# Performance work log

Hardware: AMD Instinct MI355X
Metric: run time of the kernel (lower is better)

The kernel has to match this reference:

```python
import jax, jax.numpy as jnp
import numpy as np

EPS = 1e-5

def _bn(z, g, b):
    # train-mode BatchNorm2d: batch stats over (B,H,W), biased variance
    mean = z.mean(axis=(0, 2, 3), keepdims=True)
    var = z.var(axis=(0, 2, 3), keepdims=True)
    return g[None, :, None, None] * (z - mean) * jax.lax.rsqrt(var + EPS) + b[None, :, None, None]

def _conv1x1(x, w):
    # x: [B,C,H,W], w: [O,C] -> [B,O,H,W]
    return jnp.einsum('bchw,oc->bohw', x, w)

def _proj(x, w1, g1, b1, w2, g2, b2):
    z = _bn(_conv1x1(x, w1), g1, b1)
    return _bn(_conv1x1(z, w2), g2, b2)

def setup_inputs() -> dict:
    key = jax.random.key(0)
    ks = jax.random.split(key, 24)
    B, Cx, Cy, M, H, W = 4, 512, 256, 64, 64, 64
    f32 = jnp.float32
    def wmat(k, o, c):
        return jax.random.normal(k, (o, c), f32) * (c ** -0.5)
    def gamma(k, c):
        return 1.0 + 0.1 * jax.random.normal(k, (c,), f32)
    def beta(k, c):
        return 0.1 * jax.random.normal(k, (c,), f32)
    inp = {
        'x': jax.random.normal(ks[0], (B, Cx, H, W), f32),
        'y': jax.random.normal(ks[1], (B, Cy, H, W), f32),
        # f_self
        'ws1': wmat(ks[2], M, Cx), 'gs1': gamma(ks[3], M), 'bs1': beta(ks[4], M),
        'ws2': wmat(ks[5], M, M),  'gs2': gamma(ks[6], M), 'bs2': beta(ks[7], M),
        # f_x
        'wx1': wmat(ks[8], M, Cx), 'gx1': gamma(ks[9], M), 'bx1': beta(ks[10], M),
        'wx2': wmat(ks[11], M, M), 'gx2': gamma(ks[12], M), 'bx2': beta(ks[13], M),
        # f_y
        'wy1': wmat(ks[14], M, Cy), 'gy1': gamma(ks[15], M), 'by1': beta(ks[16], M),
        'wy2': wmat(ks[17], M, M),  'gy2': gamma(ks[18], M), 'by2': beta(ks[19], M),
        # f_up
        'wu': wmat(ks[20], Cx, M), 'gu': gamma(ks[21], Cx), 'bu': beta(ks[22], Cx),
    }
    return inp

def reference(x, y, ws1, gs1, bs1, ws2, gs2, bs2,
              wx1, gx1, bx1, wx2, gx2, bx2,
              wy1, gy1, by1, wy2, gy2, by2,
              wu, gu, bu):
    B, C, H, W = x.shape
    M = ws1.shape[0]
    N = H * W
    fself = _proj(x, ws1, gs1, bs1, ws2, gs2, bs2).reshape(B, M, N).transpose(0, 2, 1)  # [B,N,M]
    fx = _proj(x, wx1, gx1, bx1, wx2, gx2, bx2).reshape(B, M, N).transpose(0, 2, 1)      # [B,N,M]
    fy = _proj(y, wy1, gy1, by1, wy2, gy2, by2).reshape(B, M, N)                          # [B,M,N]
    sim = jnp.matmul(fx, fy)                  # [B,N,N]  (scale=False)
    attn = jax.nn.softmax(sim, axis=-1)
    fout = jnp.matmul(attn, fself)            # [B,N,M]
    fout = fout.transpose(0, 2, 1).reshape(B, M, H, W)
    out = _bn(_conv1x1(fout, wu), gu, bu)
    return x + out
```

## Files before the change

kernel.cpp:

```cpp
#include <hip/hip_runtime.h>
#include <hip/hip_fp16.h>
#include <cstdint>

constexpr int N_ = 4096;
constexpr float CNT = 16384.f;

typedef __attribute__((ext_vector_type(8))) _Float16 half8;
typedef __attribute__((ext_vector_type(4))) float f32x4;
union fragh { half8 h8; int i4[4]; };

__device__ inline int pkh(float a, float b) {
  union { __half2 h; int i; } u;
  u.h = __float22half2_rn(float2{a, b});
  return u.i;
}


__global__ __launch_bounds__(256) void conv1_k(
    const float* __restrict__ x, const float* __restrict__ y,
    const float* __restrict__ ws1, const float* __restrict__ wx1,
    const float* __restrict__ wy1,
    float* __restrict__ z1s, float* __restrict__ z1x, float* __restrict__ z1y,
    float* __restrict__ stats) {
  const int t = threadIdx.x;
  const int slice = blockIdx.x;
  const int b = slice >> 5;
  const int n0 = (slice & 31) * 128;
  const int branch = blockIdx.y;
  const float* A = branch == 2 ? y : x;
  const float* W = branch == 0 ? ws1 : (branch == 1 ? wx1 : wy1);
  float* out = branch == 0 ? z1s : (branch == 1 ? z1x : z1y);
  const int K = branch == 2 ? 256 : 512;
  float* st = stats + branch * 128;

  __shared__ float sA[32][132];
  __shared__ float sW[32][72];

  const int to = (t >> 5) * 8;
  const int tn = (t & 31) * 4;
  float acc[8][4];
#pragma unroll
  for (int i = 0; i < 8; ++i)
#pragma unroll
    for (int j = 0; j < 4; ++j) acc[i][j] = 0.f;

  const float* Ab = A + (size_t)b * K * N_ + n0;
#pragma unroll 1
  for (int k0 = 0; k0 < K; k0 += 32) {
    __syncthreads();
#pragma unroll
    for (int i = 0; i < 4; ++i) {
      int row = i * 8 + (t >> 5);
      float4 v = *(const float4*)&Ab[(size_t)(k0 + row) * N_ + tn];
      *(float4*)&sA[row][tn] = v;
    }
    {
      int o = t >> 2, kk = (t & 3) * 8;
      float4 w0 = *(const float4*)&W[(size_t)o * K + k0 + kk];
      float4 w1 = *(const float4*)&W[(size_t)o * K + k0 + kk + 4];
      sW[kk + 0][o] = w0.x; sW[kk + 1][o] = w0.y;
      sW[kk + 2][o] = w0.z; sW[kk + 3][o] = w0.w;
      sW[kk + 4][o] = w1.x; sW[kk + 5][o] = w1.y;
      sW[kk + 6][o] = w1.z; sW[kk + 7][o] = w1.w;
    }
    __syncthreads();
#pragma unroll
    for (int k = 0; k < 32; ++k) {
      float4 a = *(const float4*)&sA[k][tn];
      float4 w0 = *(const float4*)&sW[k][to];
      float4 w1 = *(const float4*)&sW[k][to + 4];
      float wv[8] = {w0.x, w0.y, w0.z, w0.w, w1.x, w1.y, w1.z, w1.w};
      float av[4] = {a.x, a.y, a.z, a.w};
#pragma unroll
      for (int i = 0; i < 8; ++i)
#pragma unroll
        for (int j = 0; j < 4; ++j) acc[i][j] += wv[i] * av[j];
    }
  }
  float* Cb = out + (size_t)b * 64 * N_ + n0;
#pragma unroll
  for (int i = 0; i < 8; ++i) {
    float4 v = {acc[i][0], acc[i][1], acc[i][2], acc[i][3]};
    *(float4*)&Cb[(size_t)(to + i) * N_ + tn] = v;
  }
#pragma unroll
  for (int i = 0; i < 8; ++i) {
    float s = acc[i][0] + acc[i][1] + acc[i][2] + acc[i][3];
    float q = acc[i][0] * acc[i][0] + acc[i][1] * acc[i][1] +
              acc[i][2] * acc[i][2] + acc[i][3] * acc[i][3];
#pragma unroll
    for (int d = 1; d < 32; d <<= 1) { s += __shfl_xor(s, d); q += __shfl_xor(q, d); }
    if ((t & 31) == 0) { atomicAdd(&st[to + i], s); atomicAdd(&st[64 + to + i], q); }
  }
}

__global__ __launch_bounds__(256) void conv2_k(
    const float* __restrict__ z1s, const float* __restrict__ z1x,
    const float* __restrict__ z1y,
    const float* __restrict__ ws2, const float* __restrict__ wx2,
    const float* __restrict__ wy2,
    const float* __restrict__ gs1, const float* __restrict__ bs1,
    const float* __restrict__ gx1, const float* __restrict__ bx1,
    const float* __restrict__ gy1, const float* __restrict__ by1,
    float* __restrict__ z2s, float* __restrict__ z2x, float* __restrict__ z2y,
    float* __restrict__ stats) {
  const int t = threadIdx.x;
  const int slice = blockIdx.x;
  const int b = slice >> 5;
  const int n0 = (slice & 31) * 128;
  const int branch = blockIdx.y;
  const float* A = branch == 0 ? z1s : (branch == 1 ? z1x : z1y);
  const float* W = branch == 0 ? ws2 : (branch == 1 ? wx2 : wy2);
  const float* g1 = branch == 0 ? gs1 : (branch == 1 ? gx1 : gy1);
  const float* b1 = branch == 0 ? bs1 : (branch == 1 ? bx1 : by1);
  float* out = branch == 0 ? z2s : (branch == 1 ? z2x : z2y);
  const float* stin = stats + branch * 128;
  float* stout = stats + (3 + branch) * 128;

  __shared__ float sA[32][132];
  __shared__ float sW[32][72];
  __shared__ float sc[64], sh[64];

  if (t < 64) {
    float mean = stin[t] * (1.f / CNT);
    float var = stin[64 + t] * (1.f / CNT) - mean * mean;
    float r = rsqrtf(var + 1e-5f);
    float s = g1[t] * r;
    sc[t] = s;
    sh[t] = b1[t] - mean * s;
  }

  const int to = (t >> 5) * 8;
  const int tn = (t & 31) * 4;
  float acc[8][4];
#pragma unroll
  for (int i = 0; i < 8; ++i)
#pragma unroll
    for (int j = 0; j < 4; ++j) acc[i][j] = 0.f;

  const float* Ab = A + (size_t)b * 64 * N_ + n0;
#pragma unroll 1
  for (int k0 = 0; k0 < 64; k0 += 32) {
    __syncthreads();
#pragma unroll
    for (int i = 0; i < 4; ++i) {
      int row = i * 8 + (t >> 5);
      float4 v = *(const float4*)&Ab[(size_t)(k0 + row) * N_ + tn];
      float s = sc[k0 + row], h = sh[k0 + row];
      v.x = v.x * s + h; v.y = v.y * s + h; v.z = v.z * s + h; v.w = v.w * s + h;
      *(float4*)&sA[row][tn] = v;
    }
    {
      int o = t >> 2, kk = (t & 3) * 8;
      float4 w0 = *(const float4*)&W[(size_t)o * 64 + k0 + kk];
      float4 w1 = *(const float4*)&W[(size_t)o * 64 + k0 + kk + 4];
      sW[kk + 0][o] = w0.x; sW[kk + 1][o] = w0.y;
      sW[kk + 2][o] = w0.z; sW[kk + 3][o] = w0.w;
      sW[kk + 4][o] = w1.x; sW[kk + 5][o] = w1.y;
      sW[kk + 6][o] = w1.z; sW[kk + 7][o] = w1.w;
    }
    __syncthreads();
#pragma unroll
    for (int k = 0; k < 32; ++k) {
      float4 a = *(const float4*)&sA[k][tn];
      float4 w0 = *(const float4*)&sW[k][to];
      float4 w1 = *(const float4*)&sW[k][to + 4];
      float wv[8] = {w0.x, w0.y, w0.z, w0.w, w1.x, w1.y, w1.z, w1.w};
      float av[4] = {a.x, a.y, a.z, a.w};
#pragma unroll
      for (int i = 0; i < 8; ++i)
#pragma unroll
        for (int j = 0; j < 4; ++j) acc[i][j] += wv[i] * av[j];
    }
  }
  float* Cb = out + (size_t)b * 64 * N_ + n0;
#pragma unroll
  for (int i = 0; i < 8; ++i) {
    float4 v = {acc[i][0], acc[i][1], acc[i][2], acc[i][3]};
    *(float4*)&Cb[(size_t)(to + i) * N_ + tn] = v;
  }
#pragma unroll
  for (int i = 0; i < 8; ++i) {
    float s = acc[i][0] + acc[i][1] + acc[i][2] + acc[i][3];
    float q = acc[i][0] * acc[i][0] + acc[i][1] * acc[i][1] +
              acc[i][2] * acc[i][2] + acc[i][3] * acc[i][3];
#pragma unroll
    for (int d = 1; d < 32; d <<= 1) { s += __shfl_xor(s, d); q += __shfl_xor(q, d); }
    if ((t & 31) == 0) { atomicAdd(&stout[to + i], s); atomicAdd(&stout[64 + to + i], q); }
  }
}

__global__ __launch_bounds__(256) void pack_k(
    const float* __restrict__ z2s, const float* __restrict__ z2x,
    const float* __restrict__ z2y,
    const float* __restrict__ gs2, const float* __restrict__ bs2,
    const float* __restrict__ gx2, const float* __restrict__ bx2,
    const float* __restrict__ gy2, const float* __restrict__ by2,
    int* __restrict__ Qh, int* __restrict__ Kh, int* __restrict__ Vp,
    const float* __restrict__ stats) {
  const int job = blockIdx.z;
  const int idx = blockIdx.x * 256 + threadIdx.x;
  const float* z2 = job == 0 ? z2x : (job == 1 ? z2y : z2s);
  const float* g2 = job == 0 ? gx2 : (job == 1 ? gy2 : gs2);
  const float* b2 = job == 0 ? bx2 : (job == 1 ? by2 : bs2);
  const float* st = stats + (job == 0 ? 4 : (job == 1 ? 5 : 3)) * 128;
  int* outp = job == 0 ? Qh : (job == 1 ? Kh : Vp);

  auto snorm = [&](int c, float& s, float& h) {
    float mean = st[c] * (1.f / CNT);
    float var = st[64 + c] * (1.f / CNT) - mean * mean;
    float r = rsqrtf(var + 1e-5f);
    s = g2[c] * r;
    h = b2[c] - mean * s;
  };
  if (job < 2) {
    int n = idx & 4095, c = (idx >> 12) & 31, b = idx >> 17;
    float s0, h0, s1, h1;
    snorm(2 * c, s0, h0);
    snorm(2 * c + 1, s1, h1);
    float v0 = z2[((size_t)b * 64 + 2 * c) * N_ + n] * s0 + h0;
    float v1 = z2[((size_t)b * 64 + 2 * c + 1) * N_ + n] * s1 + h1;
    outp[idx] = pkh(v0, v1);
  } else {
    int k = idx & 2047, ch = (idx >> 11) & 63, b = idx >> 17;
    float s0, h0;
    snorm(ch, s0, h0);
    float2 v = *(const float2*)&z2[((size_t)b * 64 + ch) * N_ + 2 * k];
    outp[idx] = pkh(v.x * s0 + h0, v.y * s0 + h0);
  }
}

__global__ __launch_bounds__(256) void attn_k(const int* __restrict__ Qh,
                                              const int* __restrict__ Kh,
                                              const int* __restrict__ Vp,
                                              float* __restrict__ fout) {
  const int tid = threadIdx.x;
  const int lane = tid & 63;
  const int wid = tid >> 6;
  const int la = lane & 15;
  const int quad = lane >> 4;
  const int b = blockIdx.x & 3;
  const int qbase = (blockIdx.x >> 2) * 16;
  const int* Qb = Qh + (size_t)b * 32 * N_;
  const int* Kb = Kh + (size_t)b * 32 * N_;
  const int* Vb = Vp + (size_t)b * 64 * 2048;

  __shared__ union USm {
    int P16[4][16 * 20];
    struct { float O[4][16][68]; float M[4][16]; float L[4][16]; } e;
  } smu;
  int* myP = smu.P16[wid];

  fragh aq[2];
#pragma unroll
  for (int c = 0; c < 2; ++c)
#pragma unroll
    for (int j = 0; j < 4; ++j)
      aq[c].i4[j] = Qb[(size_t)(c * 16 + quad * 4 + j) * N_ + qbase + la];

  f32x4 o[4];
  float mrun = -3.0e38f, lrun = 0.f;
#pragma unroll
  for (int mt = 0; mt < 4; ++mt) o[mt] = f32x4{0.f, 0.f, 0.f, 0.f};

  const int jbeg = wid * (N_ / 4);
#pragma unroll 1
  for (int j0 = jbeg; j0 < jbeg + N_ / 4; j0 += 32) {
    f32x4 s[2];
#pragma unroll
    for (int nt = 0; nt < 2; ++nt) {
      fragh k0, k1;
      const int key = j0 + nt * 16 + la;
#pragma unroll
      for (int jj = 0; jj < 4; ++jj) {
        k0.i4[jj] = Kb[(size_t)(quad * 4 + jj) * N_ + key];
        k1.i4[jj] = Kb[(size_t)(16 + quad * 4 + jj) * N_ + key];
      }
      f32x4 z = f32x4{0.f, 0.f, 0.f, 0.f};
      z = __builtin_amdgcn_mfma_f32_16x16x32_f16(k0.h8, aq[0].h8, z, 0, 0, 0);
      s[nt] = __builtin_amdgcn_mfma_f32_16x16x32_f16(k1.h8, aq[1].h8, z, 0, 0, 0);
    }
    float t0 = fmaxf(fmaxf(s[0][0], s[0][1]), fmaxf(s[0][2], s[0][3]));
    float t1 = fmaxf(fmaxf(s[1][0], s[1][1]), fmaxf(s[1][2], s[1][3]));
    float t = fmaxf(t0, t1);
    t = fmaxf(t, __shfl_xor(t, 16));
    t = fmaxf(t, __shfl_xor(t, 32));
    float mnew = fmaxf(mrun, t);
    float alpha = __expf(mrun - mnew);
    float p[2][4];
    float ps = 0.f;
#pragma unroll
    for (int nt = 0; nt < 2; ++nt)
#pragma unroll
      for (int r = 0; r < 4; ++r) {
        p[nt][r] = __expf(s[nt][r] - mnew);
        ps += p[nt][r];
      }
    ps += __shfl_xor(ps, 16);
    ps += __shfl_xor(ps, 32);
    lrun = lrun * alpha + ps;
    mrun = mnew;
#pragma unroll
    for (int nt = 0; nt < 2; ++nt) {
      myP[(nt * 8 + quad * 2 + 0) * 20 + la] = pkh(p[nt][0], p[nt][1]);
      myP[(nt * 8 + quad * 2 + 1) * 20 + la] = pkh(p[nt][2], p[nt][3]);
    }
    __asm__ __volatile__("s_waitcnt lgkmcnt(0)" ::: "memory");
    fragh pb;
#pragma unroll
    for (int j = 0; j < 4; ++j) pb.i4[j] = myP[(quad * 4 + j) * 20 + la];
#pragma unroll
    for (int mt = 0; mt < 4; ++mt) {
      o[mt][0] *= alpha; o[mt][1] *= alpha;
      o[mt][2] *= alpha; o[mt][3] *= alpha;
    }
#pragma unroll
    for (int mt = 0; mt < 4; ++mt) {
      const int4 vv = *(const int4*)&Vb[(size_t)(mt * 16 + la) * 2048 + (j0 >> 1) + quad * 4];
      fragh vb;
      vb.i4[0] = vv.x; vb.i4[1] = vv.y; vb.i4[2] = vv.z; vb.i4[3] = vv.w;
      o[mt] = __builtin_amdgcn_mfma_f32_16x16x32_f16(vb.h8, pb.h8, o[mt], 0, 0, 0);
    }
  }

  __syncthreads();
  if (quad == 0) {
    smu.e.M[wid][la] = mrun;
    smu.e.L[wid][la] = lrun;
  }
#pragma unroll
  for (int mt = 0; mt < 4; ++mt)
#pragma unroll
    for (int r = 0; r < 4; ++r) smu.e.O[wid][la][mt * 16 + quad * 4 + r] = o[mt][r];
  __syncthreads();

#pragma unroll
  for (int t = 0; t < 4; ++t) {
    int oidx = t * 256 + tid;
    int m = oidx >> 4;
    int q = oidx & 15;
    float m0 = fmaxf(fmaxf(smu.e.M[0][q], smu.e.M[1][q]),
                     fmaxf(smu.e.M[2][q], smu.e.M[3][q]));
    float num = 0.f, den = 0.f;
#pragma unroll
    for (int w = 0; w < 4; ++w) {
      float wgt = __expf(smu.e.M[w][q] - m0);
      num += wgt * smu.e.O[w][q][m];
      den += wgt * smu.e.L[w][q];
    }
    fout[((size_t)b * 64 + m) * N_ + qbase + q] = num / den;
  }
}

__global__ __launch_bounds__(256) void convup_k(const float* __restrict__ fout,
                                                const float* __restrict__ wu,
                                                float* __restrict__ u,
                                                float* __restrict__ stats) {
  const int t = threadIdx.x;
  const int slice = blockIdx.x;
  const int b = slice >> 5;
  const int n0 = (slice & 31) * 128;
  const int o0 = blockIdx.y * 64;

  __shared__ float sA[32][132];
  __shared__ float sW[32][72];

  const int to = (t >> 5) * 8;
  const int tn = (t & 31) * 4;
  float acc[8][4];
#pragma unroll
  for (int i = 0; i < 8; ++i)
#pragma unroll
    for (int j = 0; j < 4; ++j) acc[i][j] = 0.f;

  const float* Ab = fout + (size_t)b * 64 * N_ + n0;
#pragma unroll 1
  for (int k0 = 0; k0 < 64; k0 += 32) {
    __syncthreads();
#pragma unroll
    for (int i = 0; i < 4; ++i) {
      int row = i * 8 + (t >> 5);
      float4 v = *(const float4*)&Ab[(size_t)(k0 + row) * N_ + tn];
      *(float4*)&sA[row][tn] = v;
    }
    {
      int o = t >> 2, kk = (t & 3) * 8;
      float4 w0 = *(const float4*)&wu[(size_t)(o0 + o) * 64 + k0 + kk];
      float4 w1 = *(const float4*)&wu[(size_t)(o0 + o) * 64 + k0 + kk + 4];
      sW[kk + 0][o] = w0.x; sW[kk + 1][o] = w0.y;
      sW[kk + 2][o] = w0.z; sW[kk + 3][o] = w0.w;
      sW[kk + 4][o] = w1.x; sW[kk + 5][o] = w1.y;
      sW[kk + 6][o] = w1.z; sW[kk + 7][o] = w1.w;
    }
    __syncthreads();
#pragma unroll
    for (int k = 0; k < 32; ++k) {
      float4 a = *(const float4*)&sA[k][tn];
      float4 w0 = *(const float4*)&sW[k][to];
      float4 w1 = *(const float4*)&sW[k][to + 4];
      float wv[8] = {w0.x, w0.y, w0.z, w0.w, w1.x, w1.y, w1.z, w1.w};
      float av[4] = {a.x, a.y, a.z, a.w};
#pragma unroll
      for (int i = 0; i < 8; ++i)
#pragma unroll
        for (int j = 0; j < 4; ++j) acc[i][j] += wv[i] * av[j];
    }
  }
  float* Cb = u + ((size_t)b * 512 + o0) * N_ + n0;
#pragma unroll
  for (int i = 0; i < 8; ++i) {
    float4 v = {acc[i][0], acc[i][1], acc[i][2], acc[i][3]};
    *(float4*)&Cb[(size_t)(to + i) * N_ + tn] = v;
  }
#pragma unroll
  for (int i = 0; i < 8; ++i) {
    float s = acc[i][0] + acc[i][1] + acc[i][2] + acc[i][3];
    float q = acc[i][0] * acc[i][0] + acc[i][1] * acc[i][1] +
              acc[i][2] * acc[i][2] + acc[i][3] * acc[i][3];
#pragma unroll
    for (int d = 1; d < 32; d <<= 1) { s += __shfl_xor(s, d); q += __shfl_xor(q, d); }
    if ((t & 31) == 0) {
      atomicAdd(&stats[768 + o0 + to + i], s);
      atomicAdd(&stats[1280 + o0 + to + i], q);
    }
  }
}

__global__ __launch_bounds__(256) void final_k(const float* __restrict__ x,
                                               const float* __restrict__ u,
                                               const float* __restrict__ gu,
                                               const float* __restrict__ bu,
                                               const float* __restrict__ stats,
                                               float* __restrict__ out) {
  size_t idx = (size_t)blockIdx.x * 256 + threadIdx.x;
  int c = (int)((idx >> 12) & 511);
  float mean = stats[768 + c] * (1.f / CNT);
  float var = stats[1280 + c] * (1.f / CNT) - mean * mean;
  float r = rsqrtf(var + 1e-5f);
  float s = gu[c] * r;
  float sh = bu[c] - mean * s;
  out[idx] = x[idx] + u[idx] * s + sh;
}

extern "C" void kernel_launch(void* const* d_in, const int* in_sizes, int n_in,
                              void* d_out, int out_size, void* d_ws, size_t ws_size,
                              hipStream_t stream) {
  const float* x = (const float*)d_in[0];
  const float* y = (const float*)d_in[1];
  const float* ws1 = (const float*)d_in[2];
  const float* gs1 = (const float*)d_in[3];
  const float* bs1 = (const float*)d_in[4];
  const float* ws2 = (const float*)d_in[5];
  const float* gs2 = (const float*)d_in[6];
  const float* bs2 = (const float*)d_in[7];
  const float* wx1 = (const float*)d_in[8];
  const float* gx1 = (const float*)d_in[9];
  const float* bx1 = (const float*)d_in[10];
  const float* wx2 = (const float*)d_in[11];
  const float* gx2 = (const float*)d_in[12];
  const float* bx2 = (const float*)d_in[13];
  const float* wy1 = (const float*)d_in[14];
  const float* gy1 = (const float*)d_in[15];
  const float* by1 = (const float*)d_in[16];
  const float* wy2 = (const float*)d_in[17];
  const float* gy2 = (const float*)d_in[18];
  const float* by2 = (const float*)d_in[19];
  const float* wu = (const float*)d_in[20];
  const float* gu = (const float*)d_in[21];
  const float* bu = (const float*)d_in[22];
  float* out = (float*)d_out;

  float* w = (float*)d_ws;
  const size_t M1 = 1048576;
  float* z1s = w + 0 * M1;
  float* z1x = w + 1 * M1;
  float* z1y = w + 2 * M1;
  float* z2s = w + 3 * M1;
  float* z2x = w + 4 * M1;
  float* z2y = w + 5 * M1;
  float* fout = w + 6 * M1;
  float* u = w + 7 * M1;
  int* Qh = (int*)(w + 15 * M1);
  int* Kh = Qh + 524288;
  int* Vp = Kh + 524288;
  float* stats = (float*)(Vp + 524288);

  hipMemsetAsync(stats, 0, 1792 * sizeof(float), stream);

  conv1_k<<<dim3(128, 3), dim3(256), 0, stream>>>(x, y, ws1, wx1, wy1, z1s, z1x,
                                                  z1y, stats);
  conv2_k<<<dim3(128, 3), dim3(256), 0, stream>>>(
      z1s, z1x, z1y, ws2, wx2, wy2, gs1, bs1, gx1, bx1, gy1, by1, z2s, z2x, z2y,
      stats);
  pack_k<<<dim3(2048, 1, 3), dim3(256), 0, stream>>>(z2s, z2x, z2y, gs2, bs2, gx2,
                                                     bx2, gy2, by2, Qh, Kh, Vp,
                                                     stats);
  attn_k<<<dim3(1024), dim3(256), 0, stream>>>(Qh, Kh, Vp, fout);
  convup_k<<<dim3(128, 8), dim3(256), 0, stream>>>(fout, wu, u, stats);
  final_k<<<dim3(32768), dim3(256), 0, stream>>>(x, u, gu, bu, stats, out);
}
```

Measured before the change: 400.5 us.

## Pre-swizzle K/V into MFMA fragment order and software-pipeline K loads

The pack kernel now writes K and V in the exact per-lane MFMA fragment layout, so the attention kernel loads each operand with one contiguous int4 per lane instead of strided scalar gathers. The attention loop is unrolled by two with double-buffered K registers, prefetching the next K tile and issuing the V loads before the softmax math so global latency overlaps compute. It also adds a minimum-occupancy launch bound and pads the shared epilogue buffer to reduce bank conflicts. The cost is more register pressure and scattered writes in the pack kernel.

```diff
diff --git a/kernel.cpp b/kernel.cpp
--- a/kernel.cpp
+++ b/kernel.cpp
@@ -196,7 +196,7 @@
     const float* __restrict__ gs2, const float* __restrict__ bs2,
     const float* __restrict__ gx2, const float* __restrict__ bx2,
     const float* __restrict__ gy2, const float* __restrict__ by2,
-    int* __restrict__ Qh, int* __restrict__ Kh, int* __restrict__ Vp,
+    int* __restrict__ Qh, int* __restrict__ Kf, int* __restrict__ Vf,
     const float* __restrict__ stats) {
   const int job = blockIdx.z;
   const int idx = blockIdx.x * 256 + threadIdx.x;
@@ -204,7 +204,7 @@
   const float* g2 = job == 0 ? gx2 : (job == 1 ? gy2 : gs2);
   const float* b2 = job == 0 ? bx2 : (job == 1 ? by2 : bs2);
   const float* st = stats + (job == 0 ? 4 : (job == 1 ? 5 : 3)) * 128;
-  int* outp = job == 0 ? Qh : (job == 1 ? Kh : Vp);
+  int* outp = job == 0 ? Qh : (job == 1 ? Kf : Vf);
 
   auto snorm = [&](int c, float& s, float& h) {
     float mean = st[c] * (1.f / CNT);
@@ -213,7 +213,7 @@
     s = g2[c] * r;
     h = b2[c] - mean * s;
   };
-  if (job < 2) {
+  if (job == 0) {
     int n = idx & 4095, c = (idx >> 12) & 31, b = idx >> 17;
     float s0, h0, s1, h1;
     snorm(2 * c, s0, h0);
@@ -221,19 +221,30 @@
     float v0 = z2[((size_t)b * 64 + 2 * c) * N_ + n] * s0 + h0;
     float v1 = z2[((size_t)b * 64 + 2 * c + 1) * N_ + n] * s1 + h1;
     outp[idx] = pkh(v0, v1);
+  } else if (job == 1) {
+    int n = idx & 4095, c = (idx >> 12) & 31, b = idx >> 17;
+    float s0, h0, s1, h1;
+    snorm(2 * c, s0, h0);
+    snorm(2 * c + 1, s1, h1);
+    float v0 = z2[((size_t)b * 64 + 2 * c) * N_ + n] * s0 + h0;
+    float v1 = z2[((size_t)b * 64 + 2 * c + 1) * N_ + n] * s1 + h1;
+    int t16 = n >> 4, la = n & 15, g = c >> 4, quad = (c & 15) >> 2, jj = c & 3;
+    outp[(((b * 256 + t16) * 2 + g) * 64 + quad * 16 + la) * 4 + jj] = pkh(v0, v1);
   } else {
     int k = idx & 2047, ch = (idx >> 11) & 63, b = idx >> 17;
     float s0, h0;
     snorm(ch, s0, h0);
     float2 v = *(const float2*)&z2[((size_t)b * 64 + ch) * N_ + 2 * k];
-    outp[idx] = pkh(v.x * s0 + h0, v.y * s0 + h0);
-  }
-}
-
-__global__ __launch_bounds__(256) void attn_k(const int* __restrict__ Qh,
-                                              const int* __restrict__ Kh,
-                                              const int* __restrict__ Vp,
-                                              float* __restrict__ fout) {
+    int kb = k >> 4, p = k & 15, quad = p >> 2, w = p & 3, mt = ch >> 4, la = ch & 15;
+    outp[(((b * 128 + kb) * 4 + mt) * 64 + quad * 16 + la) * 4 + w] =
+        pkh(v.x * s0 + h0, v.y * s0 + h0);
+  }
+}
+
+__global__ __launch_bounds__(256, 4) void attn_k(const int* __restrict__ Qh,
+                                                 const int* __restrict__ Kf,
+                                                 const int* __restrict__ Vf,
+                                                 float* __restrict__ fout) {
   const int tid = threadIdx.x;
   const int lane = tid & 63;
   const int wid = tid >> 6;
@@ -242,12 +253,12 @@
   const int b = blockIdx.x & 3;
   const int qbase = (blockIdx.x >> 2) * 16;
   const int* Qb = Qh + (size_t)b * 32 * N_;
-  const int* Kb = Kh + (size_t)b * 32 * N_;
-  const int* Vb = Vp + (size_t)b * 64 * 2048;
+  const int* Kb4 = Kf + (size_t)b * 131072;
+  const int* Vb4 = Vf + (size_t)b * 131072;
 
   __shared__ union USm {
     int P16[4][16 * 20];
-    struct { float O[4][16][68]; float M[4][16]; float L[4][16]; } e;
+    struct { float O[4][16][69]; float M[4][16]; float L[4][16]; } e;
   } smu;
   int* myP = smu.P16[wid];
 
@@ -264,22 +275,38 @@
   for (int mt = 0; mt < 4; ++mt) o[mt] = f32x4{0.f, 0.f, 0.f, 0.f};
 
   const int jbeg = wid * (N_ / 4);
-#pragma unroll 1
-  for (int j0 = jbeg; j0 < jbeg + N_ / 4; j0 += 32) {
+  const int jend = jbeg + N_ / 4;
+
+  int4 ka[2][2], kb2[2][2];
+#pragma unroll
+  for (int nt = 0; nt < 2; ++nt)
+#pragma unroll
+    for (int g = 0; g < 2; ++g)
+      ka[nt][g] = *(const int4*)&Kb4[((((jbeg >> 4) + nt) * 2 + g) * 64 + lane) * 4];
+
+  auto body = [&](int j0, int4 (&kc)[2][2], int4 (&kn)[2][2]) {
     f32x4 s[2];
 #pragma unroll
     for (int nt = 0; nt < 2; ++nt) {
       fragh k0, k1;
-      const int key = j0 + nt * 16 + la;
-#pragma unroll
-      for (int jj = 0; jj < 4; ++jj) {
-        k0.i4[jj] = Kb[(size_t)(quad * 4 + jj) * N_ + key];
-        k1.i4[jj] = Kb[(size_t)(16 + quad * 4 + jj) * N_ + key];
-      }
+      k0.i4[0] = kc[nt][0].x; k0.i4[1] = kc[nt][0].y;
+      k0.i4[2] = kc[nt][0].z; k0.i4[3] = kc[nt][0].w;
+      k1.i4[0] = kc[nt][1].x; k1.i4[1] = kc[nt][1].y;
+      k1.i4[2] = kc[nt][1].z; k1.i4[3] = kc[nt][1].w;
       f32x4 z = f32x4{0.f, 0.f, 0.f, 0.f};
       z = __builtin_amdgcn_mfma_f32_16x16x32_f16(k0.h8, aq[0].h8, z, 0, 0, 0);
       s[nt] = __builtin_amdgcn_mfma_f32_16x16x32_f16(k1.h8, aq[1].h8, z, 0, 0, 0);
     }
+    int4 vv[4];
+#pragma unroll
+    for (int mt = 0; mt < 4; ++mt)
+      vv[mt] = *(const int4*)&Vb4[(((j0 >> 5) * 4 + mt) * 64 + lane) * 4];
+    const int nj = (j0 + 32 < jend) ? (j0 + 32) : jbeg;
+#pragma unroll
+    for (int nt = 0; nt < 2; ++nt)
+#pragma unroll
+      for (int g = 0; g < 2; ++g)
+        kn[nt][g] = *(const int4*)&Kb4[((((nj >> 4) + nt) * 2 + g) * 64 + lane) * 4];
     float t0 = fmaxf(fmaxf(s[0][0], s[0][1]), fmaxf(s[0][2], s[0][3]));
     float t1 = fmaxf(fmaxf(s[1][0], s[1][1]), fmaxf(s[1][2], s[1][3]));
     float t = fmaxf(t0, t1);
@@ -316,11 +343,17 @@
     }
 #pragma unroll
     for (int mt = 0; mt < 4; ++mt) {
-      const int4 vv = *(const int4*)&Vb[(size_t)(mt * 16 + la) * 2048 + (j0 >> 1) + quad * 4];
       fragh vb;
-      vb.i4[0] = vv.x; vb.i4[1] = vv.y; vb.i4[2] = vv.z; vb.i4[3] = vv.w;
+      vb.i4[0] = vv[mt].x; vb.i4[1] = vv[mt].y;
+      vb.i4[2] = vv[mt].z; vb.i4[3] = vv[mt].w;
       o[mt] = __builtin_amdgcn_mfma_f32_16x16x32_f16(vb.h8, pb.h8, o[mt], 0, 0, 0);
     }
+  };
+
+#pragma unroll 1
+  for (int j0 = jbeg; j0 < jend; j0 += 64) {
+    body(j0, ka, kb2);
+    body(j0 + 32, kb2, ka);
   }
 
   __syncthreads();
@@ -481,9 +514,9 @@
   float* fout = w + 6 * M1;
   float* u = w + 7 * M1;
   int* Qh = (int*)(w + 15 * M1);
-  int* Kh = Qh + 524288;
-  int* Vp = Kh + 524288;
-  float* stats = (float*)(Vp + 524288);
+  int* Kf = Qh + 524288;
+  int* Vf = Kf + 524288;
+  float* stats = (float*)(Vf + 524288);
 
   hipMemsetAsync(stats, 0, 1792 * sizeof(float), stream);
 
@@ -493,9 +526,9 @@
       z1s, z1x, z1y, ws2, wx2, wy2, gs1, bs1, gx1, bx1, gy1, by1, z2s, z2x, z2y,
       stats);
   pack_k<<<dim3(2048, 1, 3), dim3(256), 0, stream>>>(z2s, z2x, z2y, gs2, bs2, gx2,
-                                                     bx2, gy2, by2, Qh, Kh, Vp,
+                                                     bx2, gy2, by2, Qh, Kf, Vf,
                                                      stats);
-  attn_k<<<dim3(1024), dim3(256), 0, stream>>>(Qh, Kh, Vp, fout);
+  attn_k<<<dim3(1024), dim3(256), 0, stream>>>(Qh, Kf, Vf, fout);
   convup_k<<<dim3(128, 8), dim3(256), 0, stream>>>(fout, wu, u, stats);
   final_k<<<dim3(32768), dim3(256), 0, stream>>>(x, u, gu, bu, stats, out);
 }
```

Result: faster. 365.8 us (-8.7%).
